# Optimization experiments

Measured on AMD Instinct MI355X. Metric: run time of the kernel, lower is better.

## Reference

```python
import jax, jax.numpy as jnp
import numpy as np

N_NODES = 100000
N_CAND = 32768
HIDDEN = 1024
N_REL = 10


def setup_inputs() -> dict:
    key = jax.random.key(0)
    k0, k1, k2, k3, k4, k5 = jax.random.split(key, 6)
    node_embeddings = jax.random.normal(k0, (N_NODES, HIDDEN), dtype=jnp.float32)
    src_idx = jax.random.randint(k1, (N_CAND,), 0, N_NODES, dtype=jnp.int32)
    dst_idx = jax.random.randint(k2, (N_CAND,), 0, N_NODES, dtype=jnp.int32)
    labels = jax.random.randint(k3, (N_CAND,), 0, N_REL, dtype=jnp.int32)
    # Linear weights stored as [in, out] so forward is x @ W + b
    W1 = jax.random.normal(k4, (4 * HIDDEN, HIDDEN), dtype=jnp.float32) * (1.0 / np.sqrt(4 * HIDDEN))
    b1 = jnp.zeros((HIDDEN,), dtype=jnp.float32)
    W2 = jax.random.normal(k5, (HIDDEN, N_REL), dtype=jnp.float32) * (1.0 / np.sqrt(HIDDEN))
    b2 = jnp.zeros((N_REL,), dtype=jnp.float32)
    return {"node_embeddings": node_embeddings, "src_idx": src_idx, "dst_idx": dst_idx,
            "labels": labels, "W1": W1, "b1": b1, "W2": W2, "b2": b2}


def reference(node_embeddings, src_idx, dst_idx, labels, W1, b1, W2, b2):
    # Vectorized gather of candidate endpoints (replaces Python loop)
    src = node_embeddings[src_idx]            # [C, H]
    dst = node_embeddings[dst_idx]            # [C, H]
    feats = jnp.concatenate([src, dst, jnp.abs(src - dst), src * dst], axis=-1)  # [C, 4H]
    h = jax.nn.gelu(feats @ W1 + b1, approximate=False)  # exact GELU, matches torch default
    # Dropout is identity in eval mode
    logits = h @ W2 + b2                      # [C, n_rel]
    logp = jax.nn.log_softmax(logits, axis=-1)
    loss = -jnp.mean(jnp.take_along_axis(logp, labels[:, None].astype(jnp.int32), axis=-1))
    return loss, logits
```

## Files before the change

### kernel.cpp

```cpp
#include <hip/hip_runtime.h>
#include <stdint.h>

#define CANDS 32768
#define HID   1024
#define KDIM  4096
#define NREL  10

typedef __attribute__((ext_vector_type(8))) short bf16x8;
typedef __attribute__((ext_vector_type(4))) float f32x4;

__device__ __forceinline__ float bf2f(unsigned short u) {
  union { unsigned int i; float f; } v; v.i = ((unsigned int)u) << 16; return v.f;
}
__device__ __forceinline__ unsigned short f2bf(float f) {
  union { float f; unsigned int i; } v; v.f = f;
  unsigned int x = v.i;
  return (unsigned short)((x + 0x7FFFu + ((x >> 16) & 1u)) >> 16);
}
__device__ __forceinline__ void async16(const void* g, void* l) {
  __builtin_amdgcn_global_load_lds(
      (const __attribute__((address_space(1))) unsigned int*)(uintptr_t)g,
      (__attribute__((address_space(3))) unsigned int*)(uintptr_t)l,
      16, 0, 0);
}

__global__ void transpose_w1(const float* __restrict__ W1,
                             unsigned short* __restrict__ W1T) {
  __shared__ __align__(16) unsigned short tile[64][72];
  int bk = blockIdx.x;
  int bn = blockIdx.y;
  int t = threadIdx.x;
  int r = t >> 3, c8 = (t & 7) * 8;
  for (int i = 0; i < 2; ++i) {
    int rr = r + i * 32;
    const float4* src = (const float4*)(W1 + (size_t)(bk * 64 + rr) * HID + bn * 64 + c8);
    float4 v0 = src[0], v1 = src[1];
    tile[rr][c8 + 0] = f2bf(v0.x); tile[rr][c8 + 1] = f2bf(v0.y);
    tile[rr][c8 + 2] = f2bf(v0.z); tile[rr][c8 + 3] = f2bf(v0.w);
    tile[rr][c8 + 4] = f2bf(v1.x); tile[rr][c8 + 5] = f2bf(v1.y);
    tile[rr][c8 + 6] = f2bf(v1.z); tile[rr][c8 + 7] = f2bf(v1.w);
  }
  __syncthreads();
  for (int i = 0; i < 2; ++i) {
    int rr = r + i * 32;
    unsigned short tmp[8];
    for (int j = 0; j < 8; ++j) tmp[j] = tile[c8 + j][rr];
    ushort4* dst = (ushort4*)(W1T + (size_t)(bn * 64 + rr) * KDIM + bk * 64 + c8);
    dst[0] = *(ushort4*)&tmp[0];
    dst[1] = *(ushort4*)&tmp[4];
  }
}

__global__ __launch_bounds__(256) void build_feats(
    const float* __restrict__ emb,
    const int* __restrict__ sidx,
    const int* __restrict__ didx,
    unsigned short* __restrict__ feats) {
  int t = threadIdx.x;
  for (int m = blockIdx.x; m < CANDS; m += gridDim.x) {
    const float* srow = emb + (size_t)sidx[m] * HID;
    const float* drow = emb + (size_t)didx[m] * HID;
    float4 s4 = *(const float4*)(srow + t * 4);
    float4 d4 = *(const float4*)(drow + t * 4);
    unsigned short* o = feats + (size_t)m * KDIM;
    ushort4 sv, dv, av, pv;
    sv.x = f2bf(s4.x); sv.y = f2bf(s4.y); sv.z = f2bf(s4.z); sv.w = f2bf(s4.w);
    dv.x = f2bf(d4.x); dv.y = f2bf(d4.y); dv.z = f2bf(d4.z); dv.w = f2bf(d4.w);
    av.x = f2bf(fabsf(s4.x - d4.x)); av.y = f2bf(fabsf(s4.y - d4.y));
    av.z = f2bf(fabsf(s4.z - d4.z)); av.w = f2bf(fabsf(s4.w - d4.w));
    pv.x = f2bf(s4.x * d4.x); pv.y = f2bf(s4.y * d4.y);
    pv.z = f2bf(s4.z * d4.z); pv.w = f2bf(s4.w * d4.w);
    *(ushort4*)(o + t * 4)           = sv;
    *(ushort4*)(o + HID + t * 4)     = dv;
    *(ushort4*)(o + 2 * HID + t * 4) = av;
    *(ushort4*)(o + 3 * HID + t * 4) = pv;
  }
}

#define BM 128
#define BN 128
#define BK 32
__global__ __launch_bounds__(256) void gemm1_gelu(
    const unsigned short* __restrict__ A,
    const unsigned short* __restrict__ BT,
    const float* __restrict__ b1,
    unsigned short* __restrict__ H) {
  __shared__ __align__(16) unsigned short laA[BM * BK];
  __shared__ __align__(16) unsigned short laB[BN * BK];
  int bid = blockIdx.x;
  int xcd = bid & 7;
  int s   = bid >> 3;
  int m_tile = xcd * 32 + (s >> 3);
  int n_tile = s & 7;
  int m0 = m_tile * BM;
  int n0 = n_tile * BN;

  int t = threadIdx.x;
  int lane = t & 63;
  int wave = t >> 6;
  int wrow = (wave >> 1) * 64, wcol = (wave & 1) * 64;
  int quad = lane >> 4, l16 = lane & 15;

  f32x4 acc[4][4] = {};

  int srow = t >> 2;
  int scol = (t & 3) * 8;
  const unsigned short* gA0 = A  + (size_t)(m0 + srow) * KDIM + scol;
  const unsigned short* gA1 = A  + (size_t)(m0 + srow + 64) * KDIM + scol;
  const unsigned short* gB0 = BT + (size_t)(n0 + srow) * KDIM + scol;
  const unsigned short* gB1 = BT + (size_t)(n0 + srow + 64) * KDIM + scol;
  unsigned short* lA0 = &laA[srow * BK + scol];
  unsigned short* lA1 = &laA[(srow + 64) * BK + scol];
  unsigned short* lB0 = &laB[srow * BK + scol];
  unsigned short* lB1 = &laB[(srow + 64) * BK + scol];

  for (int kk = 0; kk < KDIM; kk += BK) {
    async16(gA0 + kk, lA0);
    async16(gA1 + kk, lA1);
    async16(gB0 + kk, lB0);
    async16(gB1 + kk, lB1);
    __syncthreads();
    bf16x8 af[4], bfr[4];
#pragma unroll
    for (int i = 0; i < 4; ++i)
      af[i] = *(const bf16x8*)&laA[(wrow + i * 16 + l16) * BK + quad * 8];
#pragma unroll
    for (int j = 0; j < 4; ++j)
      bfr[j] = *(const bf16x8*)&laB[(wcol + j * 16 + l16) * BK + quad * 8];
#pragma unroll
    for (int i = 0; i < 4; ++i)
#pragma unroll
      for (int j = 0; j < 4; ++j)
        acc[i][j] = __builtin_amdgcn_mfma_f32_16x16x32_bf16(af[i], bfr[j], acc[i][j], 0, 0, 0);
    __syncthreads();
  }
#pragma unroll
  for (int j = 0; j < 4; ++j) {
    int n = n0 + wcol + j * 16 + l16;
    float bias = b1[n];
#pragma unroll
    for (int i = 0; i < 4; ++i) {
#pragma unroll
      for (int r = 0; r < 4; ++r) {
        int m = m0 + wrow + i * 16 + quad * 4 + r;
        float x = acc[i][j][r] + bias;
        float g = 0.5f * x * (1.0f + erff(x * 0.70710678118654752f));
        H[(size_t)m * HID + n] = f2bf(g);
      }
    }
  }
}

__global__ __launch_bounds__(256) void gemm2_loss(
    const unsigned short* __restrict__ H,
    const float* __restrict__ W2,
    const float* __restrict__ b2,
    const int* __restrict__ labels,
    float* __restrict__ out,
    float* __restrict__ gacc) {
#define W2P 1032
  __shared__ __align__(16) unsigned short w2t[16 * W2P];
  __shared__ float lacc;
  int t = threadIdx.x;
  int lane = t & 63, wave = t >> 6;
  int quad = lane >> 4, l16 = lane & 15;
  if (t == 0) lacc = 0.0f;
  for (int k = t; k < HID; k += 256) {
    for (int j = 0; j < NREL; ++j) w2t[j * W2P + k] = f2bf(W2[(size_t)k * NREL + j]);
    for (int j = NREL; j < 16; ++j) w2t[j * W2P + k] = 0;
  }
  __syncthreads();

  int r0 = blockIdx.x * 64 + wave * 16;
  const unsigned short* hrow = H + (size_t)(r0 + l16) * HID;
  f32x4 acc = {};
#pragma unroll 8
  for (int s = 0; s < 32; ++s) {
    bf16x8 a = *(const bf16x8*)(hrow + s * 32 + quad * 8);
    bf16x8 b = *(const bf16x8*)&w2t[l16 * W2P + s * 32 + quad * 8];
    acc = __builtin_amdgcn_mfma_f32_16x16x32_bf16(a, b, acc, 0, 0, 0);
  }

  int col = l16;
  float bias = (col < NREL) ? b2[col] : 0.0f;
  float local = 0.0f;
#pragma unroll
  for (int r = 0; r < 4; ++r) {
    int row = r0 + quad * 4 + r;
    float x = acc[r] + bias;
    float v = (col < NREL) ? x : -1e30f;
    float mx = v;
    for (int d = 1; d < 16; d <<= 1) mx = fmaxf(mx, __shfl_xor(mx, d));
    float e = (col < NREL) ? expf(x - mx) : 0.0f;
    float se = e;
    for (int d = 1; d < 16; d <<= 1) se += __shfl_xor(se, d);
    float lse = mx + logf(se);
    if (col < NREL) {
      out[1 + (size_t)row * NREL + col] = x;
      if (labels[row] == col) local += (lse - x);
    }
  }
  atomicAdd(&lacc, local);
  __syncthreads();
  if (t == 0) atomicAdd(gacc, lacc);
}

__global__ void finalize_loss(const float* __restrict__ gacc, float* __restrict__ out) {
  out[0] = *gacc * (1.0f / (float)CANDS);
}

extern "C" void kernel_launch(void* const* d_in, const int* in_sizes, int n_in,
                              void* d_out, int out_size, void* d_ws, size_t ws_size,
                              hipStream_t stream) {
  const float* emb    = (const float*)d_in[0];
  const int*   sidx   = (const int*)d_in[1];
  const int*   didx   = (const int*)d_in[2];
  const int*   labels = (const int*)d_in[3];
  const float* W1     = (const float*)d_in[4];
  const float* b1     = (const float*)d_in[5];
  const float* W2     = (const float*)d_in[6];
  const float* b2     = (const float*)d_in[7];
  float* out = (float*)d_out;

  char* ws = (char*)d_ws;
  float*          gacc  = (float*)ws;
  unsigned short* W1T   = (unsigned short*)(ws + 256);
  unsigned short* feats = (unsigned short*)(ws + 256 + 8388608);
  unsigned short* H     = (unsigned short*)(ws + 256 + 8388608 + 268435456);

  hipMemsetAsync(gacc, 0, sizeof(float), stream);
  transpose_w1<<<dim3(64, 16), 256, 0, stream>>>(W1, W1T);
  build_feats<<<2048, 256, 0, stream>>>(emb, sidx, didx, feats);
  gemm1_gelu<<<2048, 256, 0, stream>>>(feats, W1T, b1, H);
  gemm2_loss<<<CANDS / 64, 256, 0, stream>>>(H, W2, b2, labels, out, gacc);
  finalize_loss<<<1, 1, 0, stream>>>(gacc, out);
}
```

Measured before the change: 951.8 us.

## Rewrite GEMM1 with 256x256 tiles, double-buffered async LDS loads and swizzle

The GEMM1 kernel moves from 128x128x32 tiles with 256 threads to 256x256x64 tiles with 512 threads (8 waves, each computing 128x64). Global-to-LDS loads are double-buffered in 128KB of dynamic shared memory, and explicit vmcnt waits let the next stage load while MFMAs run on the current one. An XOR swizzle on the K chunks avoids LDS bank conflicts, and s_setprio raises wave priority during the MFMA phase. The aim is more data reuse per LDS byte and hiding global latency that was exposed by the single-buffer, double-sync loop. The cost is higher register pressure (128 accumulator floats per thread) and heavy LDS use, which may limit occupancy to one block per CU despite the launch bound of 2.

```diff
diff --git a/kernel.cpp b/kernel.cpp
--- a/kernel.cpp
+++ b/kernel.cpp
@@ -77,78 +77,102 @@
   }
 }
 
-#define BM 128
-#define BN 128
-#define BK 32
-__global__ __launch_bounds__(256) void gemm1_gelu(
+#define G1_BM 256
+#define G1_BN 256
+#define G1_BK 64
+#define G1_NT (KDIM / G1_BK)
+
+__global__ __launch_bounds__(512, 2) void gemm1_gelu(
     const unsigned short* __restrict__ A,
     const unsigned short* __restrict__ BT,
     const float* __restrict__ b1,
     unsigned short* __restrict__ H) {
-  __shared__ __align__(16) unsigned short laA[BM * BK];
-  __shared__ __align__(16) unsigned short laB[BN * BK];
+  extern __shared__ __align__(16) unsigned short smem[];
+
   int bid = blockIdx.x;
-  int xcd = bid & 7;
-  int s   = bid >> 3;
-  int m_tile = xcd * 32 + (s >> 3);
-  int n_tile = s & 7;
-  int m0 = m_tile * BM;
-  int n0 = n_tile * BN;
-
-  int t = threadIdx.x;
-  int lane = t & 63;
-  int wave = t >> 6;
-  int wrow = (wave >> 1) * 64, wcol = (wave & 1) * 64;
+  int wg  = (bid & 7) * 64 + (bid >> 3);
+  int m0 = (wg >> 2) * G1_BM;
+  int n0 = (wg & 3) * G1_BN;
+
+  int t = threadIdx.x;
+  int lane = t & 63, w = t >> 6;
+  int wm = w >> 2, wn = w & 3;
   int quad = lane >> 4, l16 = lane & 15;
 
-  f32x4 acc[4][4] = {};
-
-  int srow = t >> 2;
-  int scol = (t & 3) * 8;
-  const unsigned short* gA0 = A  + (size_t)(m0 + srow) * KDIM + scol;
-  const unsigned short* gA1 = A  + (size_t)(m0 + srow + 64) * KDIM + scol;
-  const unsigned short* gB0 = BT + (size_t)(n0 + srow) * KDIM + scol;
-  const unsigned short* gB1 = BT + (size_t)(n0 + srow + 64) * KDIM + scol;
-  unsigned short* lA0 = &laA[srow * BK + scol];
-  unsigned short* lA1 = &laA[(srow + 64) * BK + scol];
-  unsigned short* lB0 = &laB[srow * BK + scol];
-  unsigned short* lB1 = &laB[(srow + 64) * BK + scol];
-
-  for (int kk = 0; kk < KDIM; kk += BK) {
-    async16(gA0 + kk, lA0);
-    async16(gA1 + kk, lA1);
-    async16(gB0 + kk, lB0);
-    async16(gB1 + kk, lB1);
-    __syncthreads();
-    bf16x8 af[4], bfr[4];
-#pragma unroll
-    for (int i = 0; i < 4; ++i)
-      af[i] = *(const bf16x8*)&laA[(wrow + i * 16 + l16) * BK + quad * 8];
-#pragma unroll
-    for (int j = 0; j < 4; ++j)
-      bfr[j] = *(const bf16x8*)&laB[(wcol + j * 16 + l16) * BK + quad * 8];
-#pragma unroll
-    for (int i = 0; i < 4; ++i)
+  int tr = t >> 3;
+  int slot = t & 7;
+  int gk8 = (slot ^ (tr & 7)) * 8;
+  const unsigned short* gA = A  + (size_t)(m0 + tr) * KDIM + gk8;
+  const unsigned short* gB = BT + (size_t)(n0 + tr) * KDIM + gk8;
+  int lidx = t * 8;
+
+  int sx = l16 & 7;
+  int aoff = (wm * 128 + l16) * G1_BK + ((quad ^ sx) * 8);
+  int boff = (wn * 64  + l16) * G1_BK + ((quad ^ sx) * 8);
+
+  f32x4 acc[8][4] = {};
+
+#define G1_STAGE(b, kkelem) do {                                               \
+    unsigned short* la_ = smem + (b) * 32768;                                  \
+    unsigned short* lb_ = la_ + 16384;                                         \
+    _Pragma("unroll")                                                          \
+    for (int l_ = 0; l_ < 4; ++l_)                                             \
+      async16(gA + (size_t)l_ * 64 * KDIM + (kkelem), la_ + l_ * 4096 + lidx); \
+    _Pragma("unroll")                                                          \
+    for (int l_ = 0; l_ < 4; ++l_)                                             \
+      async16(gB + (size_t)l_ * 64 * KDIM + (kkelem), lb_ + l_ * 4096 + lidx); \
+  } while (0)
+
+  G1_STAGE(0, 0);
+  for (int kt = 0; kt < G1_NT; ++kt) {
+    int c = kt & 1;
+    if (kt + 1 < G1_NT) {
+      G1_STAGE(c ^ 1, (kt + 1) * G1_BK);
+      asm volatile("s_waitcnt vmcnt(8)" ::: "memory");
+    } else {
+      asm volatile("s_waitcnt vmcnt(0)" ::: "memory");
+    }
+    __builtin_amdgcn_s_barrier();
+    asm volatile("" ::: "memory");
+    const unsigned short* bufA = smem + c * 32768;
+    const unsigned short* bufB = bufA + 16384;
+    __builtin_amdgcn_s_setprio(1);
+#pragma unroll
+    for (int h = 0; h < 2; ++h) {
+      bf16x8 bfr[4], afr[8];
 #pragma unroll
       for (int j = 0; j < 4; ++j)
-        acc[i][j] = __builtin_amdgcn_mfma_f32_16x16x32_bf16(af[i], bfr[j], acc[i][j], 0, 0, 0);
-    __syncthreads();
-  }
+        bfr[j] = *(const bf16x8*)&bufB[(boff ^ (h << 5)) + j * 1024];
+#pragma unroll
+      for (int i = 0; i < 8; ++i)
+        afr[i] = *(const bf16x8*)&bufA[(aoff ^ (h << 5)) + i * 1024];
+#pragma unroll
+      for (int i = 0; i < 8; ++i)
+#pragma unroll
+        for (int j = 0; j < 4; ++j)
+          acc[i][j] = __builtin_amdgcn_mfma_f32_16x16x32_bf16(afr[i], bfr[j], acc[i][j], 0, 0, 0);
+    }
+    __builtin_amdgcn_s_setprio(0);
+    asm volatile("" ::: "memory");
+    __builtin_amdgcn_s_barrier();
+  }
+
 #pragma unroll
   for (int j = 0; j < 4; ++j) {
-    int n = n0 + wcol + j * 16 + l16;
+    int n = n0 + wn * 64 + j * 16 + l16;
     float bias = b1[n];
 #pragma unroll
-    for (int i = 0; i < 4; ++i) {
+    for (int i = 0; i < 8; ++i) {
 #pragma unroll
       for (int r = 0; r < 4; ++r) {
-        int m = m0 + wrow + i * 16 + quad * 4 + r;
+        int m = m0 + wm * 128 + i * 16 + quad * 4 + r;
         float x = acc[i][j][r] + bias;
         float g = 0.5f * x * (1.0f + erff(x * 0.70710678118654752f));
         H[(size_t)m * HID + n] = f2bf(g);
       }
     }
   }
+#undef G1_STAGE
 }
 
 __global__ __launch_bounds__(256) void gemm2_loss(
@@ -228,10 +252,17 @@
   unsigned short* feats = (unsigned short*)(ws + 256 + 8388608);
   unsigned short* H     = (unsigned short*)(ws + 256 + 8388608 + 268435456);
 
+  static bool g1_attr_set = false;
+  if (!g1_attr_set) {
+    (void)hipFuncSetAttribute((const void*)gemm1_gelu,
+                              hipFuncAttributeMaxDynamicSharedMemorySize, 131072);
+    g1_attr_set = true;
+  }
+
   hipMemsetAsync(gacc, 0, sizeof(float), stream);
   transpose_w1<<<dim3(64, 16), 256, 0, stream>>>(W1, W1T);
   build_feats<<<2048, 256, 0, stream>>>(emb, sidx, didx, feats);
-  gemm1_gelu<<<2048, 256, 0, stream>>>(feats, W1T, b1, H);
+  gemm1_gelu<<<512, 512, 131072, stream>>>(feats, W1T, b1, H);
   gemm2_loss<<<CANDS / 64, 256, 0, stream>>>(H, W2, b2, labels, out, gacc);
   finalize_loss<<<1, 1, 0, stream>>>(gacc, out);
 }
```

After: 876.5 us. 7.9% less time.
